# Kernel tuning notes

Hardware: AMD Instinct MI355X
Metric: run time of the kernel (lower is better)

The kernel has to match this reference:

```python
import jax, jax.numpy as jnp
import numpy as np

B, S, D, H = 4, 2048, 512, 8
DK = D // H

def setup_inputs() -> dict:
    key = jax.random.key(0)
    ks = jax.random.split(key, 16)
    w = lambda i, shp: (jax.random.normal(ks[i], shp, jnp.float32) * 0.02)
    return {
        "q": jax.random.normal(ks[0], (B, S, D), jnp.float32),
        "k": jax.random.normal(ks[1], (B, S, D), jnp.float32),
        "v": jax.random.normal(ks[2], (B, S, D), jnp.float32),
        "mask": jax.random.randint(ks[3], (B, 1, S), 0, 2, jnp.int32),
        "Lexicon": jax.random.uniform(ks[4], (B, S), jnp.float32) * 1000.0,
        "Wq": w(5, (D, D)), "bq": w(6, (D,)),
        "Wk": w(7, (D, D)), "bk": w(8, (D,)),
        "Wv": w(9, (D, D)), "bv": w(10, (D,)),
        "Wo": w(11, (D, D)), "bo": w(12, (D,)),
        "Wl": w(13, (S, S)), "bl": w(14, (S,)),
    }

def reference(q, k, v, mask, Lexicon, Wq, bq, Wk, bk, Wv, bv, Wo, bo, Wl, bl):
    NEG = jnp.float32(-1e9)
    proj = lambda x, W, b: (x @ W + b).reshape(B, S, H, DK).transpose(0, 2, 1, 3)  # [B,H,S,DK]
    qh, kh, vh = proj(q, Wq, bq), proj(k, Wk, bk), proj(v, Wv, bv)
    scores = jnp.einsum('bhqd,bhkd->bhqk', qh, kh) / jnp.sqrt(jnp.float32(DK))  # [B,H,S,S]
    lex = (Lexicon / 1000.0) @ Wl + bl  # [B,S] lexicon bias over key positions
    m = mask[:, None, :, :] == 1  # [B,1,1,S]
    scores = jnp.where(m, NEG, scores)
    lexb = jnp.where(m, NEG, lex[:, None, None, :])  # [B,1,1,S]; broadcast over heads & queries
    # dropout in eval mode (identity); dual softmax then average
    attn = (jax.nn.softmax(scores, axis=-1) + jax.nn.softmax(lexb, axis=-1)) * 0.5
    out = jnp.einsum('bhqk,bhkd->bhqd', attn, vh)
    concat = out.transpose(0, 2, 1, 3).reshape(B, S, D)
    return concat @ Wo + bo
```

## Files before the change

kernel.cpp:

```cpp
#include <hip/hip_runtime.h>


typedef __attribute__((ext_vector_type(4))) float f32x4;
typedef __attribute__((ext_vector_type(8))) short s16x8;
typedef __attribute__((ext_vector_type(4))) short s16x4;

#define QSCALE 0.18033688011112042f

__device__ inline short f2bf(float f) {
  __bf16 h = (__bf16)f;
  return __builtin_bit_cast(short, h);
}
__device__ inline float fast_exp2(float x) {
#if __has_builtin(__builtin_amdgcn_exp2f)
  return __builtin_amdgcn_exp2f(x);
#else
  return exp2f(x);
#endif
}
__device__ inline void gl_lds16(const void* g, void* l) {
  __builtin_amdgcn_global_load_lds(
      (const __attribute__((address_space(1))) void*)g,
      (__attribute__((address_space(3))) void*)l, 16, 0, 0);
}

struct PrepArgs {
  const float* W[4];
  short* WT[4];
  const float* Lex;
  const float* Wl;
  float* part;
};

__global__ __launch_bounds__(256) void prep(PrepArgs pa) {
  const int blk = blockIdx.x;
  if (blk < 1024) {
    const int z = blk >> 8, tt = blk & 255;
    const float* __restrict__ W = pa.W[z];
    short* __restrict__ WT = pa.WT[z];
    const int n0 = (tt & 15) * 32, k0 = (tt >> 4) * 32;
    const int tx = threadIdx.x & 31, ty = threadIdx.x >> 5;
    __shared__ float Tl[32][33];
#pragma unroll
    for (int j = 0; j < 4; ++j)
      Tl[ty + j * 8][tx] = W[(size_t)(k0 + ty + j * 8) * 512 + n0 + tx];
    __syncthreads();
#pragma unroll
    for (int j = 0; j < 4; ++j) {
      int n = n0 + ty + j * 8, k = k0 + tx;
      int kg = k >> 3;
      int kswz = (((kg & ~7) | ((kg & 7) ^ (n & 7))) << 3) | (k & 7);
      WT[(size_t)n * 512 + kswz] = f2bf(Tl[tx][ty + j * 8]);
    }
  } else {
    const int jb = blk - 1024;
    const int j = (jb & 7) * 256 + threadIdx.x;
    const int sb = jb >> 3, s0 = sb * 128;
    __shared__ float Lsh[4][128];
#pragma unroll
    for (int l = 0; l < 2; ++l) {
      int idx = threadIdx.x + l * 256;
      Lsh[idx >> 7][idx & 127] = pa.Lex[(idx >> 7) * 2048 + s0 + (idx & 127)];
    }
    __syncthreads();
    float a0 = 0.f, a1 = 0.f, a2 = 0.f, a3 = 0.f;
#pragma unroll 4
    for (int si = 0; si < 128; ++si) {
      float w = pa.Wl[(size_t)(s0 + si) * 2048 + j];
      a0 += Lsh[0][si] * w; a1 += Lsh[1][si] * w;
      a2 += Lsh[2][si] * w; a3 += Lsh[3][si] * w;
    }
    pa.part[(sb * 4 + 0) * 2048 + j] = a0;
    pa.part[(sb * 4 + 1) * 2048 + j] = a1;
    pa.part[(sb * 4 + 2) * 2048 + j] = a2;
    pa.part[(sb * 4 + 3) * 2048 + j] = a3;
  }
}

__global__ __launch_bounds__(256) void vbar2(const float* __restrict__ t1p,
                                             const float* __restrict__ psp,
                                             const float* __restrict__ Wv,
                                             const float* __restrict__ bv,
                                             float* __restrict__ vbar) {
  const int b = blockIdx.x, jb = blockIdx.y, tid = threadIdx.x;
  const int jl = tid & 63, sp = tid >> 6;
  const int j = jb * 64 + jl;
  __shared__ float t1[512];
  __shared__ float red[4][64];
#pragma unroll
  for (int l = 0; l < 2; ++l) {
    int idx = tid + l * 256;
    float s = 0.f;
#pragma unroll 8
    for (int p = 0; p < 64; ++p) s += t1p[(size_t)(b * 64 + p) * 512 + idx];
    t1[idx] = s;
  }
  __syncthreads();
  float a = 0.f;
#pragma unroll 4
  for (int d = sp * 128; d < sp * 128 + 128; ++d) a += t1[d] * Wv[(size_t)d * 512 + j];
  red[sp][jl] = a;
  __syncthreads();
  if (sp == 0) {
    float tot = 0.f;
#pragma unroll 8
    for (int p = 0; p < 64; ++p) tot += psp[b * 64 + p];
    float s = red[0][jl] + red[1][jl] + red[2][jl] + red[3][jl];
    vbar[b * 512 + j] = s / tot + bv[j];
  }
}

struct GemmArgs {
  const void* X[3];
  const short* WT[3];
  const float* bias[3];
  void* C[3];
  float oscale[3];
  int mode[3];
  const int* mask;
  const float* part;
  const float* bl;
  const float* vsrc;
  float* t1p;
  float* psp;
};

template <bool IN_F32>
__global__ __launch_bounds__(256) void gemm_fused(GemmArgs ga) {
  constexpr int LDA = IN_F32 ? 72 : 64;
  __shared__ alignas(16) short SH[64 * 72 + 128 * 64];
  const int tid = threadIdx.x;

  if (blockIdx.z == 3) {
    const int id2 = blockIdx.y * 128 + blockIdx.x;
    if (id2 >= 256) return;
    float* ek = (float*)SH;
    const int b = id2 >> 6, kb = id2 & 63;
    if (tid < 32) {
      int k = kb * 32 + tid;
      float s = 0.f;
#pragma unroll
      for (int sb = 0; sb < 16; ++sb) s += ga.part[(sb * 4 + b) * 2048 + k];
      float lx = s * 0.001f + ga.bl[k];
      ek[tid] = (ga.mask[b * 2048 + k] == 1) ? 0.f : __expf(lx);
    }
    __syncthreads();
    float a0 = 0.f, a1 = 0.f;
#pragma unroll 4
    for (int kk = 0; kk < 32; ++kk) {
      float e = ek[kk];
      const float* vr = ga.vsrc + (size_t)(b * 2048 + kb * 32 + kk) * 512;
      a0 += e * vr[tid];
      a1 += e * vr[tid + 256];
    }
    ga.t1p[(size_t)id2 * 512 + tid] = a0;
    ga.t1p[(size_t)id2 * 512 + tid + 256] = a1;
    if (tid == 0) {
      float s = 0.f;
      for (int i = 0; i < 32; ++i) s += ek[i];
      ga.psp[id2] = s;
    }
    return;
  }

  short* Al = SH;
  short* Bl = SH + 64 * LDA;
  const int t = blockIdx.z;
  const short* __restrict__ WT = ga.WT[t];
  const float* __restrict__ bias = ga.bias[t];
  const int lane = tid & 63, wid = tid >> 6;
  const int lr = lane & 15, lg = lane >> 4;
  const int wm = wid >> 1, wn = wid & 1;
  const int bid = blockIdx.y * 128 + blockIdx.x;
  const int swz = ((bid & 7) << 6) | (bid >> 3);
  const int m0 = (swz >> 2) * 64, n0 = (swz & 3) * 128;
  const int grow = lane >> 3, gch = lane & 7;

  f32x4 acc[2][4];
#pragma unroll
  for (int i = 0; i < 2; ++i)
#pragma unroll
    for (int j = 0; j < 4; ++j) acc[i][j] = {0.f, 0.f, 0.f, 0.f};

  for (int k0 = 0; k0 < 512; k0 += 64) {
    __syncthreads();
    if constexpr (IN_F32) {
      const float* X = (const float*)ga.X[t];
#pragma unroll
      for (int ii = 0; ii < 4; ++ii) {
        int fidx = tid + ii * 256;
        int row = fidx >> 4, kq = fidx & 15;
        f32x4 vv = *(const f32x4*)(X + (size_t)(m0 + row) * 512 + k0 + kq * 4);
        s16x4 hv = {f2bf(vv[0]), f2bf(vv[1]), f2bf(vv[2]), f2bf(vv[3])};
        *(s16x4*)(&Al[row * 72 + kq * 4]) = hv;
      }
    } else {
      const short* X = (const short*)ga.X[t];
#pragma unroll
      for (int c = 0; c < 2; ++c) {
        int r0 = wid * 16 + c * 8;
        int row = r0 + grow;
        gl_lds16(X + (size_t)(m0 + row) * 512 + k0 + ((gch ^ (row & 7)) << 3),
                 &Al[r0 * 64]);
      }
    }
#pragma unroll
    for (int c = 0; c < 4; ++c) {
      int r0 = wid * 32 + c * 8;
      int row = r0 + grow;
      gl_lds16(WT + (size_t)(n0 + row) * 512 + k0 + (gch << 3), &Bl[r0 * 64]);
    }
    __syncthreads();
#pragma unroll
    for (int ks = 0; ks < 2; ++ks) {
      s16x8 a[2], bfr[4];
#pragma unroll
      for (int mt = 0; mt < 2; ++mt) {
        int m = wm * 32 + mt * 16 + lr;
        if constexpr (IN_F32)
          a[mt] = *(const s16x8*)(&Al[m * 72 + ks * 32 + lg * 8]);
        else
          a[mt] = *(const s16x8*)(&Al[m * 64 + (((ks * 4 + lg) ^ (m & 7)) << 3)]);
      }
#pragma unroll
      for (int nt = 0; nt < 4; ++nt) {
        int n = wn * 64 + nt * 16 + lr;
        bfr[nt] = *(const s16x8*)(&Bl[n * 64 + (((ks * 4 + lg) ^ (n & 7)) << 3)]);
      }
#pragma unroll
      for (int mt = 0; mt < 2; ++mt)
#pragma unroll
        for (int nt = 0; nt < 4; ++nt)
          acc[mt][nt] = __builtin_amdgcn_mfma_f32_16x16x32_bf16(a[mt], bfr[nt],
                                                                acc[mt][nt], 0, 0, 0);
    }
  }
  const float os = ga.oscale[t];
  const int mode = ga.mode[t];
  if (mode == 1) {
    __syncthreads();
    short* Tt = SH;
#pragma unroll
    for (int nt = 0; nt < 4; ++nt) {
      int dl = wn * 64 + nt * 16 + lr;
      float bvv = bias[n0 + dl];
#pragma unroll
      for (int mt = 0; mt < 2; ++mt) {
        int sl = wm * 32 + mt * 16 + lg * 4;
#pragma unroll
        for (int i = 0; i < 4; ++i) {
          float mf = (ga.mask[m0 + sl + i] == 1) ? 0.f : 1.f;
          Tt[dl * 72 + sl + i] = f2bf((acc[mt][nt][i] + bvv) * mf);
        }
      }
    }
    __syncthreads();
    const int dl = tid >> 1, sh = (tid & 1) * 32;
    const int n = n0 + dl;
    const size_t base =
        ((size_t)((m0 >> 11) * 8 + (n >> 6)) * 64 + (n & 63)) * 2048 +
        (m0 & 2047) + sh;
#pragma unroll
    for (int c = 0; c < 4; ++c)
      *(s16x8*)((short*)ga.C[t] + base + c * 8) =
          *(const s16x8*)(&Tt[dl * 72 + sh + c * 8]);
  } else {
#pragma unroll
    for (int nt = 0; nt < 4; ++nt) {
      int col = n0 + wn * 64 + nt * 16 + lr;
      float bvv = bias[col];
#pragma unroll
      for (int mt = 0; mt < 2; ++mt) {
        int r0 = m0 + wm * 32 + mt * 16 + lg * 4;
        if (mode == 2) {
#pragma unroll
          for (int i = 0; i < 4; ++i)
            ((float*)ga.C[t])[(size_t)(r0 + i) * 512 + col] = acc[mt][nt][i] + bvv;
        } else {
#pragma unroll
          for (int i = 0; i < 4; ++i)
            ((short*)ga.C[t])[(size_t)(r0 + i) * 512 + col] =
                f2bf((acc[mt][nt][i] + bvv) * os);
        }
      }
    }
  }
}

__global__ __launch_bounds__(256) void flash_attn(const short* __restrict__ Qp,
                                                  const short* __restrict__ Kp,
                                                  const short* __restrict__ Vt,
                                                  const int* __restrict__ mask,
                                                  const float* __restrict__ vbar,
                                                  short* __restrict__ concat) {
  constexpr int S = 2048;
  __shared__ alignas(16) short Kl[2][64 * 64];
  __shared__ alignas(16) short Vl[2][64 * 64];
  __shared__ alignas(16) short Pl[4][32 * 64];
  __shared__ alignas(16) short Mb[2][64];
  const int id = blockIdx.x;
  const int xcd = id & 7, iw = id >> 3;
  const int bh = xcd * 4 + (iw >> 4), qb = iw & 15;
  const int b = bh >> 3, h = bh & 7;
  const int q0 = qb * 128;
  const int tid = threadIdx.x;
  const int lane = tid & 63, wid = tid >> 6;
  const int lr = lane & 15, lg = lane >> 4;

  const int row0 = tid >> 3, row1 = (tid + 256) >> 3, sg = tid & 7;
  const short* Kg0 = Kp + ((size_t)(b * S) + row0) * 512 + h * 64 + ((sg ^ (row0 & 7)) << 3);
  const short* Kg1 = Kp + ((size_t)(b * S) + row1) * 512 + h * 64 + ((sg ^ (row1 & 7)) << 3);
  const short* Vg0 = Vt + ((size_t)(bh * 64) + row0) * 2048 + ((sg ^ (row0 & 7)) << 3);
  const short* Vg1 = Vt + ((size_t)(bh * 64) + row1) * 2048 + ((sg ^ (row1 & 7)) << 3);

  gl_lds16(Kg0, &Kl[0][tid * 8]);
  gl_lds16(Kg1, &Kl[0][(tid + 256) * 8]);
  gl_lds16(Vg0, &Vl[0][tid * 8]);
  gl_lds16(Vg1, &Vl[0][(tid + 256) * 8]);
  if (tid < 64) Mb[0][tid] = (mask[b * S + tid] == 1) ? (short)0 : (short)0x3F80;

  const short* Qb0 = Qp + ((size_t)(b * S) + q0 + wid * 32 + lr) * 512 + h * 64;
  s16x8 aq0[2], aq1[2];
#pragma unroll
  for (int qh = 0; qh < 2; ++qh) {
    aq0[qh] = *(const s16x8*)(Qb0 + (size_t)qh * 16 * 512 + lg * 8);
    aq1[qh] = *(const s16x8*)(Qb0 + (size_t)qh * 16 * 512 + 32 + lg * 8);
  }

  f32x4 acc[2][4];
#pragma unroll
  for (int qh = 0; qh < 2; ++qh)
#pragma unroll
    for (int i = 0; i < 4; ++i) acc[qh][i] = {0.f, 0.f, 0.f, 0.f};
  f32x4 accL[2] = {{0.f, 0.f, 0.f, 0.f}, {0.f, 0.f, 0.f, 0.f}};
  const f32x4 zero = {0.f, 0.f, 0.f, 0.f};

  __syncthreads();

  int cur = 0;
  for (int t = 0; t < 32; ++t) {
    const int nxt = cur ^ 1;
    int mnxt = 0;
    if (t < 31) {
      const size_t kv0n = (size_t)(t + 1) * 64;
      gl_lds16(Kg0 + kv0n * 512, &Kl[nxt][tid * 8]);
      gl_lds16(Kg1 + kv0n * 512, &Kl[nxt][(tid + 256) * 8]);
      gl_lds16(Vg0 + kv0n, &Vl[nxt][tid * 8]);
      gl_lds16(Vg1 + kv0n, &Vl[nxt][(tid + 256) * 8]);
      if (tid < 64) mnxt = mask[b * S + kv0n + tid];
    }
    f32x4 st[2][4];
#pragma unroll
    for (int nt = 0; nt < 4; ++nt) {
      const int rbase = (nt * 16 + lr) * 64;
      s16x8 k0f = *(const s16x8*)(&Kl[cur][rbase + ((lg ^ (lr & 7)) << 3)]);
      s16x8 k1f = *(const s16x8*)(&Kl[cur][rbase + (((4 + lg) ^ (lr & 7)) << 3)]);
#pragma unroll
      for (int qh = 0; qh < 2; ++qh) {
        f32x4 tt = __builtin_amdgcn_mfma_f32_16x16x32_bf16(k0f, aq0[qh], zero, 0, 0, 0);
        st[qh][nt] = __builtin_amdgcn_mfma_f32_16x16x32_bf16(k1f, aq1[qh], tt, 0, 0, 0);
      }
    }
#pragma unroll
    for (int qh = 0; qh < 2; ++qh) {
      const int prow = (qh * 16 + lr) * 64;
#pragma unroll
      for (int nt = 0; nt < 4; ++nt) {
        float p0 = fast_exp2(st[qh][nt][0]);
        float p1 = fast_exp2(st[qh][nt][1]);
        float p2 = fast_exp2(st[qh][nt][2]);
        float p3 = fast_exp2(st[qh][nt][3]);
        s16x4 pk = {f2bf(p0), f2bf(p1), f2bf(p2), f2bf(p3)};
        int g = nt * 2 + (lg >> 1);
        *(s16x4*)(&Pl[wid][prow + ((g ^ (lr & 7)) << 3) + ((lg & 1) << 2)]) = pk;
      }
    }
#pragma unroll
    for (int ks = 0; ks < 2; ++ks) {
      const int fg = (((ks * 4 + lg) ^ (lr & 7)) << 3);
      s16x8 bm = *(const s16x8*)(&Mb[cur][ks * 32 + lg * 8]);
      s16x8 ap[2];
#pragma unroll
      for (int qh = 0; qh < 2; ++qh) {
        ap[qh] = *(const s16x8*)(&Pl[wid][(qh * 16 + lr) * 64 + fg]);
        accL[qh] = __builtin_amdgcn_mfma_f32_16x16x32_bf16(ap[qh], bm, accL[qh], 0, 0, 0);
      }
#pragma unroll
      for (int dt = 0; dt < 4; ++dt) {
        s16x8 bv = *(const s16x8*)(&Vl[cur][(dt * 16 + lr) * 64 + fg]);
#pragma unroll
        for (int qh = 0; qh < 2; ++qh)
          acc[qh][dt] = __builtin_amdgcn_mfma_f32_16x16x32_bf16(ap[qh], bv, acc[qh][dt], 0, 0, 0);
      }
    }
    if (t < 31 && tid < 64)
      Mb[nxt][tid] = (mnxt == 1) ? (short)0 : (short)0x3F80;
    __syncthreads();
    cur = nxt;
  }
#pragma unroll
  for (int qh = 0; qh < 2; ++qh) {
    f32x4 linv;
#pragma unroll
    for (int i = 0; i < 4; ++i) linv[i] = 0.5f / accL[qh][i];
#pragma unroll
    for (int dt = 0; dt < 4; ++dt) {
      int d = dt * 16 + lr;
      float vb = 0.5f * vbar[bh * 64 + d];
#pragma unroll
      for (int i = 0; i < 4; ++i) {
        int q = q0 + wid * 32 + qh * 16 + lg * 4 + i;
        concat[((size_t)(b * S) + q) * 512 + h * 64 + d] =
            f2bf(acc[qh][dt][i] * linv[i] + vb);
      }
    }
  }
}

extern "C" void kernel_launch(void* const* d_in, const int* in_sizes, int n_in,
                              void* d_out, int out_size, void* d_ws, size_t ws_size,
                              hipStream_t stream) {
  const float* q    = (const float*)d_in[0];
  const float* k    = (const float*)d_in[1];
  const float* v    = (const float*)d_in[2];
  const int*   mask = (const int*)d_in[3];
  const float* Lex  = (const float*)d_in[4];
  const float* Wq   = (const float*)d_in[5];
  const float* bq   = (const float*)d_in[6];
  const float* Wk   = (const float*)d_in[7];
  const float* bk   = (const float*)d_in[8];
  const float* Wv   = (const float*)d_in[9];
  const float* bv   = (const float*)d_in[10];
  const float* Wo   = (const float*)d_in[11];
  const float* bo   = (const float*)d_in[12];
  const float* Wl   = (const float*)d_in[13];
  const float* bl   = (const float*)d_in[14];
  float* out = (float*)d_out;

  char* ws = (char*)d_ws;
  const size_t TSZ = (size_t)8192 * 512 * 2;
  short* Qp  = (short*)(ws);
  short* Kp  = (short*)(ws + TSZ);
  short* Vtp = (short*)(ws + 2 * TSZ);
  short* Cc  = (short*)(ws + 3 * TSZ);
  float* part = (float*)(ws + 3 * TSZ);
  float* t1p  = (float*)(ws + 3 * TSZ + (512 << 10));
  short* WTq = (short*)(ws + 4 * TSZ);
  short* WTk = WTq + 512 * 512;
  short* WTv = WTk + 512 * 512;
  short* WTo = WTv + 512 * 512;
  float* psp   = (float*)(ws + 4 * TSZ + 4 * 512 * 512 * 2);
  float* vbarp = psp + 256;

  PrepArgs pa;
  pa.W[0] = Wq; pa.W[1] = Wk; pa.W[2] = Wv; pa.W[3] = Wo;
  pa.WT[0] = WTq; pa.WT[1] = WTk; pa.WT[2] = WTv; pa.WT[3] = WTo;
  pa.Lex = Lex; pa.Wl = Wl; pa.part = part;
  prep<<<1152, 256, 0, stream>>>(pa);

  GemmArgs gqkv;
  gqkv.X[0] = q;   gqkv.X[1] = k;   gqkv.X[2] = v;
  gqkv.WT[0] = WTq; gqkv.WT[1] = WTk; gqkv.WT[2] = WTv;
  gqkv.bias[0] = bq; gqkv.bias[1] = bk; gqkv.bias[2] = bv;
  gqkv.C[0] = Qp; gqkv.C[1] = Kp; gqkv.C[2] = Vtp;
  gqkv.oscale[0] = QSCALE; gqkv.oscale[1] = 1.f; gqkv.oscale[2] = 1.f;
  gqkv.mode[0] = 0; gqkv.mode[1] = 0; gqkv.mode[2] = 1;
  gqkv.mask = mask;
  gqkv.part = part; gqkv.bl = bl; gqkv.vsrc = v;
  gqkv.t1p = t1p; gqkv.psp = psp;
  gemm_fused<true><<<dim3(128, 4, 4), 256, 0, stream>>>(gqkv);

  vbar2<<<dim3(4, 8), 256, 0, stream>>>(t1p, psp, Wv, bv, vbarp);

  flash_attn<<<512, 256, 0, stream>>>(Qp, Kp, Vtp, mask, vbarp, Cc);

  GemmArgs go;
  go.X[0] = Cc; go.WT[0] = WTo; go.bias[0] = bo; go.C[0] = out;
  go.oscale[0] = 1.f; go.mode[0] = 2;
  go.X[1] = nullptr; go.WT[1] = nullptr; go.bias[1] = nullptr; go.C[1] = nullptr;
  go.X[2] = nullptr; go.WT[2] = nullptr; go.bias[2] = nullptr; go.C[2] = nullptr;
  go.oscale[1] = go.oscale[2] = 1.f; go.mode[1] = go.mode[2] = 0;
  go.mask = mask;
  go.part = nullptr; go.bl = nullptr; go.vsrc = nullptr;
  go.t1p = nullptr; go.psp = nullptr;
  gemm_fused<false><<<dim3(128, 4, 1), 256, 0, stream>>>(go);
}
```

Before: 122.8 us.

## Keep softmax probabilities in registers using 16x16x16 MFMA, drop LDS P staging

The exponentiated score tile now feeds the PV and row-sum MFMAs directly from registers. The S accumulator layout matches the A-operand layout of the 16x16x16 bf16 instruction, which removes the LDS write/read round trip through the Pl buffer and frees its shared memory. In exchange it issues twice as many smaller MFMAs (K=16 instead of K=32), with narrower 8-byte V and mask loads from LDS. That can lower matrix-core throughput per instruction.

```diff
diff --git a/kernel.cpp b/kernel.cpp
--- a/kernel.cpp
+++ b/kernel.cpp
@@ -6,6 +6,7 @@
 typedef __attribute__((ext_vector_type(4))) short s16x4;
 
 #define QSCALE 0.18033688011112042f
+#define MFMA16(a, b, c) __builtin_amdgcn_mfma_f32_16x16x16bf16_1k(a, b, c, 0, 0, 0)
 
 __device__ inline short f2bf(float f) {
   __bf16 h = (__bf16)f;
@@ -296,7 +297,6 @@
   constexpr int S = 2048;
   __shared__ alignas(16) short Kl[2][64 * 64];
   __shared__ alignas(16) short Vl[2][64 * 64];
-  __shared__ alignas(16) short Pl[4][32 * 64];
   __shared__ alignas(16) short Mb[2][64];
   const int id = blockIdx.x;
   const int xcd = id & 7, iw = id >> 3;
@@ -362,35 +362,21 @@
       }
     }
 #pragma unroll
-    for (int qh = 0; qh < 2; ++qh) {
-      const int prow = (qh * 16 + lr) * 64;
-#pragma unroll
-      for (int nt = 0; nt < 4; ++nt) {
-        float p0 = fast_exp2(st[qh][nt][0]);
-        float p1 = fast_exp2(st[qh][nt][1]);
-        float p2 = fast_exp2(st[qh][nt][2]);
-        float p3 = fast_exp2(st[qh][nt][3]);
-        s16x4 pk = {f2bf(p0), f2bf(p1), f2bf(p2), f2bf(p3)};
-        int g = nt * 2 + (lg >> 1);
-        *(s16x4*)(&Pl[wid][prow + ((g ^ (lr & 7)) << 3) + ((lg & 1) << 2)]) = pk;
-      }
-    }
-#pragma unroll
-    for (int ks = 0; ks < 2; ++ks) {
-      const int fg = (((ks * 4 + lg) ^ (lr & 7)) << 3);
-      s16x8 bm = *(const s16x8*)(&Mb[cur][ks * 32 + lg * 8]);
-      s16x8 ap[2];
-#pragma unroll
-      for (int qh = 0; qh < 2; ++qh) {
-        ap[qh] = *(const s16x8*)(&Pl[wid][(qh * 16 + lr) * 64 + fg]);
-        accL[qh] = __builtin_amdgcn_mfma_f32_16x16x32_bf16(ap[qh], bm, accL[qh], 0, 0, 0);
-      }
+    for (int nt = 0; nt < 4; ++nt) {
+      s16x4 pa0 = {f2bf(fast_exp2(st[0][nt][0])), f2bf(fast_exp2(st[0][nt][1])),
+                   f2bf(fast_exp2(st[0][nt][2])), f2bf(fast_exp2(st[0][nt][3]))};
+      s16x4 pa1 = {f2bf(fast_exp2(st[1][nt][0])), f2bf(fast_exp2(st[1][nt][1])),
+                   f2bf(fast_exp2(st[1][nt][2])), f2bf(fast_exp2(st[1][nt][3]))};
+      s16x4 bm = *(const s16x4*)(&Mb[cur][nt * 16 + lg * 4]);
+      accL[0] = MFMA16(pa0, bm, accL[0]);
+      accL[1] = MFMA16(pa1, bm, accL[1]);
 #pragma unroll
       for (int dt = 0; dt < 4; ++dt) {
-        s16x8 bv = *(const s16x8*)(&Vl[cur][(dt * 16 + lr) * 64 + fg]);
-#pragma unroll
-        for (int qh = 0; qh < 2; ++qh)
-          acc[qh][dt] = __builtin_amdgcn_mfma_f32_16x16x32_bf16(ap[qh], bv, acc[qh][dt], 0, 0, 0);
+        const int row = dt * 16 + lr;
+        const int gsw = (nt * 2 + (lg >> 1)) ^ (row & 7);
+        s16x4 bv = *(const s16x4*)(&Vl[cur][row * 64 + (gsw << 3) + ((lg & 1) << 2)]);
+        acc[0][dt] = MFMA16(pa0, bv, acc[0][dt]);
+        acc[1][dt] = MFMA16(pa1, bv, acc[1][dt]);
       }
     }
     if (t < 31 && tid < 64)
```

After: 130.6 us. 1.06x slower.
